# Kernel optimization log

Measured on AMD Instinct MI355X. Metric: run time of the kernel, lower is better.

## Reference

```python
import jax, jax.numpy as jnp
import numpy as np

B, S, D, H, T = 16, 512, 512, 8, 8
DK = D // H
SCALE = float(1.0 / np.sqrt(DK))
EPS = 1e-5


def setup_inputs() -> dict:
    key = jax.random.key(0)
    ks = jax.random.split(key, 12)
    s = float(1.0 / np.sqrt(D))  # torch Linear default init scale
    u = lambda k, shp: jax.random.uniform(k, shp, jnp.float32, -s, s)
    return {
        "x": jax.random.normal(ks[0], (B, S, D), jnp.float32),
        "x_type": jax.random.randint(ks[1], (B, S), 0, T, jnp.int32),
        "mask": jax.random.randint(ks[2], (B, S, S), 0, 2, jnp.int32),
        "Wq": u(ks[3], (T, D, D)), "bq": u(ks[4], (T, D)),
        "Wk": u(ks[5], (T, D, D)), "bk": u(ks[6], (T, D)),
        "Wv": u(ks[7], (T, D, D)), "bv": u(ks[8], (T, D)),
        "Wa": u(ks[9], (T, D, D)), "ba": u(ks[10], (T, D)),
        "gamma": jnp.ones((T, D), jnp.float32),
        "beta": jnp.zeros((T, D), jnp.float32),
    }


def _typed_proj(xf, t, W, b):
    # per-node-type linear 'experts': compute all T projections, select by type id
    # xf: [N, D], W: [T, D, D], b: [T, D], t: [N] -> [N, D]
    all_p = jnp.einsum('nd,tdh->nth', xf, W) + b[None]  # [N, T, D]
    return jnp.take_along_axis(all_p, t[:, None, None], axis=1)[:, 0]


def reference(x, x_type, mask, Wq, bq, Wk, bk, Wv, bv, Wa, ba, gamma, beta):
    xf = x.reshape(-1, D)          # [N, D], N = B*S
    t = x_type.reshape(-1)         # [N]

    # heterogeneous Q/K/V dispatch
    q = _typed_proj(xf, t, Wq, bq).reshape(B, S, H, DK).transpose(0, 2, 1, 3)
    k = _typed_proj(xf, t, Wk, bk).reshape(B, S, H, DK).transpose(0, 2, 1, 3)
    v = _typed_proj(xf, t, Wv, bv).reshape(B, S, H, DK).transpose(0, 2, 1, 3)

    # scaled dot-product attention with boolean mask (mask==0 -> -1e9)
    scores = jnp.einsum('bhqd,bhkd->bhqk', q, k) * SCALE  # [B, H, S, S]
    scores = jnp.where(mask[:, None] == 0, jnp.float32(-1e9), scores)
    p = jax.nn.softmax(scores, axis=-1)
    att = jnp.einsum('bhqk,bhkd->bhqd', p, v)             # [B, H, S, DK]
    att = att.transpose(0, 2, 1, 3).reshape(-1, D)        # [N, D]

    # per-type output projection + residual + per-type LayerNorm
    a = _typed_proj(att, t, Wa, ba)
    h = a + xf
    mu = jnp.mean(h, axis=-1, keepdims=True)
    var = jnp.mean((h - mu) ** 2, axis=-1, keepdims=True)
    out = (h - mu) * jax.lax.rsqrt(var + EPS) * gamma[t] + beta[t]
    return out.reshape(B, S, D)
```

## Files before the change

### kernel.cpp

```cpp
#include <hip/hip_runtime.h>
#include <hip/hip_bf16.h>

typedef __attribute__((ext_vector_type(8))) short short8;
typedef __attribute__((ext_vector_type(4))) float f32x4;
typedef __attribute__((ext_vector_type(4))) unsigned short u16x4;
typedef unsigned short u16;
typedef unsigned int u32;
typedef unsigned long long u64;

#define NB 16
#define NS 512
#define ND 512
#define NH 8
#define NT 8
#define NDK 64
#define NN (NB*NS)
#define SCALE_LOG2E 0.18033688011112042f
#define BM 128
#define BN 128
#define BKK 64

__device__ __forceinline__ u16 f2bf(float f) {
    __hip_bfloat16 h = __float2bfloat16(f);
    return *reinterpret_cast<u16*>(&h);
}
__device__ __forceinline__ u32 pk2(float lo, float hi) {
    return (u32)f2bf(lo) | ((u32)f2bf(hi) << 16);
}

typedef const __attribute__((address_space(1))) void* gas_t;
typedef __attribute__((address_space(3))) void* las_t;

__device__ __forceinline__ void gload16(const void* gsrc, void* ldst) {
    __builtin_amdgcn_global_load_lds((gas_t)gsrc, (las_t)ldst, 16, 0, 0);
}

__global__ __launch_bounds__(256) void bucketize(
    const int* __restrict__ xty, int* __restrict__ perm, int* __restrict__ typeoff,
    int* __restrict__ tile_type, int* __restrict__ tile_row0, int* __restrict__ ntiles)
{
    __shared__ int cnt[NT], off[NT + 1], cur[NT];
    int tid = threadIdx.x;
    if (tid < NT) cnt[tid] = 0;
    __syncthreads();
    for (int n = tid; n < NN; n += 256) atomicAdd(&cnt[xty[n]], 1);
    __syncthreads();
    if (tid == 0) {
        int acc = 0, nt = 0;
        for (int t = 0; t < NT; ++t) {
            off[t] = acc;
            for (int r = 0; r < cnt[t]; r += BM) { tile_type[nt] = t; tile_row0[nt] = acc + r; ++nt; }
            acc += cnt[t];
        }
        off[NT] = acc;
        *ntiles = nt;
        for (int t = 0; t <= NT; ++t) typeoff[t] = off[t];
    }
    __syncthreads();
    if (tid < NT) cur[tid] = off[tid];
    __syncthreads();
    for (int n = tid; n < NN; n += 256) {
        int t = xty[n];
        int p = atomicAdd(&cur[t], 1);
        perm[p] = n;
    }
}

__global__ __launch_bounds__(256) void cvt_x(const float* __restrict__ x, u16* __restrict__ xb)
{
    int i = blockIdx.x * 256 + threadIdx.x;
    float4 v = reinterpret_cast<const float4*>(x)[i];
    u16x4 o;
    o.x = f2bf(v.x); o.y = f2bf(v.y); o.z = f2bf(v.z); o.w = f2bf(v.w);
    reinterpret_cast<u16x4*>(xb)[i] = o;
}

__global__ __launch_bounds__(256) void cvt_w(
    const float* __restrict__ Wq, const float* __restrict__ Wk,
    const float* __restrict__ Wv, const float* __restrict__ Wa,
    u16* __restrict__ Wqt, u16* __restrict__ Wkt, u16* __restrict__ Wvt, u16* __restrict__ Wat)
{
    int arr = blockIdx.z >> 3, t = blockIdx.z & 7;
    const float* W = (arr == 0 ? Wq : arr == 1 ? Wk : arr == 2 ? Wv : Wa) + ((size_t)t << 18);
    u16* O = (arr == 0 ? Wqt : arr == 1 ? Wkt : arr == 2 ? Wvt : Wat) + ((size_t)t << 18);
    int d0 = blockIdx.x * 64, h0 = blockIdx.y * 64;
    __shared__ __align__(16) float tile[64][68];
    int tx = threadIdx.x & 15, ty = threadIdx.x >> 4;
    #pragma unroll
    for (int i = 0; i < 4; ++i) {
        int r = ty + i * 16;
        float4 v = *reinterpret_cast<const float4*>(&W[(size_t)(d0 + r) * ND + h0 + tx * 4]);
        *reinterpret_cast<float4*>(&tile[r][tx * 4]) = v;
    }
    __syncthreads();
    #pragma unroll
    for (int i = 0; i < 4; ++i) {
        int r = ty + i * 16;
        u16x4 o;
        o.x = f2bf(tile[tx * 4 + 0][r]);
        o.y = f2bf(tile[tx * 4 + 1][r]);
        o.z = f2bf(tile[tx * 4 + 2][r]);
        o.w = f2bf(tile[tx * 4 + 3][r]);
        *reinterpret_cast<u16x4*>(&O[(size_t)(h0 + r) * ND + d0 + tx * 4]) = o;
    }
}

__global__ __launch_bounds__(256) void pack_mask(const int* __restrict__ mask, u64* __restrict__ maskb)
{
    int i = blockIdx.x * 256 + threadIdx.x;
    int v = mask[i];
    u64 bal = __ballot(v != 0);
    if ((threadIdx.x & 63) == 0) maskb[i >> 6] = bal;
}

__global__ __launch_bounds__(256) void qkv_gemm(
    const u16* __restrict__ xb,
    const u16* __restrict__ Wqt, const u16* __restrict__ Wkt, const u16* __restrict__ Wvt,
    const float* __restrict__ bq, const float* __restrict__ bk, const float* __restrict__ bv,
    const int* __restrict__ perm, const int* __restrict__ typeoff,
    const int* __restrict__ tile_type, const int* __restrict__ tile_row0, const int* __restrict__ ntiles,
    u16* __restrict__ qb, u16* __restrict__ kbf, u16* __restrict__ vb)
{
    int work = (blockIdx.x & 7) * 108 + (blockIdx.x >> 3);
    int tile = work / 12, pc = work % 12;
    if (tile >= *ntiles) return;
    int t = tile_type[tile];
    int row0 = tile_row0[tile];
    int rows = typeoff[t + 1] - row0; if (rows > BM) rows = BM;
    int proj = pc >> 2;
    int col0 = (pc & 3) * BN;
    const u16* W = (proj == 0 ? Wqt : proj == 1 ? Wkt : Wvt) + ((size_t)t << 18);
    const float* bias = (proj == 0 ? bq : proj == 1 ? bk : bv) + (t << 9);
    u16* outp = proj == 0 ? qb : proj == 1 ? kbf : vb;
    float qscale = proj == 0 ? SCALE_LOG2E : 1.f;

    __shared__ __align__(16) u16 As[2][BM][BKK];
    __shared__ __align__(16) u16 Bs[2][BM][BKK];
    __shared__ int stok[BM];

    int tid = threadIdx.x;
    if (tid < BM) stok[tid] = perm[row0 + (tid < rows ? tid : 0)];
    __syncthreads();

    int lane = tid & 63, w = tid >> 6;
    int wr = w >> 1, wc = w & 1;
    int fr = lane & 15, g = lane >> 4;

    int lrow = lane >> 3;
    int schunk = (lane & 7) ^ lrow;
    int tokA[4];
    #pragma unroll
    for (int k = 0; k < 4; ++k) tokA[k] = stok[w * 32 + k * 8 + lrow];

    auto stage = [&](int buf, int k0) {
        #pragma unroll
        for (int k = 0; k < 4; ++k) {
            gload16(xb + (((size_t)tokA[k]) << 9) + k0 + schunk * 8, &As[buf][w * 32 + k * 8][0]);
            gload16(W + (((size_t)(col0 + w * 32 + k * 8 + lrow)) << 9) + k0 + schunk * 8,
                    &Bs[buf][w * 32 + k * 8][0]);
        }
    };

    f32x4 acc[4][4] = {};

    stage(0, 0);
    #pragma unroll
    for (int it = 0; it < 8; ++it) {
        int cur = it & 1;
        if (it < 7) {
            stage(cur ^ 1, (it + 1) * BKK);
            asm volatile("s_waitcnt vmcnt(8)" ::: "memory");
        } else {
            asm volatile("s_waitcnt vmcnt(0)" ::: "memory");
        }
        __builtin_amdgcn_s_barrier();

        const char* Ab = (const char*)As[cur];
        const char* Bb = (const char*)Bs[cur];
        #pragma unroll
        for (int ks = 0; ks < 2; ++ks) {
            short8 af[4], bfr[4];
            #pragma unroll
            for (int m = 0; m < 4; ++m) {
                int r = wr * 64 + m * 16 + fr;
                af[m] = *reinterpret_cast<const short8*>(Ab + r * 128 + (((ks * 4 + g) ^ (r & 7)) << 4));
            }
            #pragma unroll
            for (int n = 0; n < 4; ++n) {
                int r = wc * 64 + n * 16 + fr;
                bfr[n] = *reinterpret_cast<const short8*>(Bb + r * 128 + (((ks * 4 + g) ^ (r & 7)) << 4));
            }
            #pragma unroll
            for (int m = 0; m < 4; ++m)
                #pragma unroll
                for (int n = 0; n < 4; ++n)
                    acc[m][n] = __builtin_amdgcn_mfma_f32_16x16x32_bf16(af[m], bfr[n], acc[m][n], 0, 0, 0);
        }
        asm volatile("s_waitcnt lgkmcnt(0)" ::: "memory");
        __builtin_amdgcn_s_barrier();
    }

    int rbase = g << 2;
    #pragma unroll
    for (int n = 0; n < 4; ++n) {
        int c = col0 + wc * 64 + n * 16 + fr;
        float bv_ = bias[c];
        int h = c >> 6, dk = c & 63;
        #pragma unroll
        for (int m = 0; m < 4; ++m) {
            #pragma unroll
            for (int i = 0; i < 4; ++i) {
                int r = wr * 64 + m * 16 + rbase + i;
                if (r < rows) {
                    int tok = stok[r];
                    int b = tok >> 9, s = tok & 511;
                    outp[((size_t)((b * NH + h) * NS + s) << 6) + dk] =
                        f2bf((acc[m][n][i] + bv_) * qscale);
                }
            }
        }
    }
}

__global__ __launch_bounds__(256) void transp_v(const u16* __restrict__ vb, u16* __restrict__ vtb)
{
    int bh = blockIdx.y, s0 = blockIdx.x * 64;
    __shared__ __align__(16) u16 t[64][72];
    int tid = threadIdx.x;
    const u16* src = vb + ((size_t)bh << 15) + ((size_t)s0 << 6);
    #pragma unroll
    for (int it = 0; it < 2; ++it) {
        int idx = it * 256 + tid;
        int s = idx & 63, c = idx >> 6;
        short8 v = *reinterpret_cast<const short8*>(src + ((size_t)s << 6) + c * 8);
        #pragma unroll
        for (int j = 0; j < 8; ++j) t[c * 8 + j][s] = ((const u16*)&v)[j];
    }
    __syncthreads();
    u16* dst = vtb + ((size_t)bh << 15) + s0;
    #pragma unroll
    for (int it = 0; it < 2; ++it) {
        int idx = it * 256 + tid;
        int dk = idx >> 3, c = idx & 7;
        short8 v = *reinterpret_cast<const short8*>(&t[dk][c * 8]);
        *reinterpret_cast<short8*>(dst + (size_t)dk * NS + c * 8) = v;
    }
}

__global__ __launch_bounds__(256) void attn_mfma(
    const u16* __restrict__ qb, const u16* __restrict__ kbf, const u16* __restrict__ vtb,
    const u64* __restrict__ maskb, u16* __restrict__ attb)
{
    int work = (blockIdx.x & 7) * 128 + (blockIdx.x >> 3);
    int bh = work >> 3, jq = work & 7;
    int b = bh >> 3, h = bh & 7;
    int q0 = jq * 64;
    int tid = threadIdx.x, lane = tid & 63, w = tid >> 6;
    int ln15 = lane & 15, g = lane >> 4;

    __shared__ __align__(16) u16 sK[64 * 64];
    __shared__ __align__(16) u16 sVt[64 * 64];
    __shared__ __align__(16) u16 sP[4 * 16 * 68];

    const u16* Qg = qb + ((size_t)(bh * NS + q0 + w * 16 + ln15) << 6);
    short8 aq0 = *reinterpret_cast<const short8*>(Qg + g * 8);
    short8 aq1 = *reinterpret_cast<const short8*>(Qg + 32 + g * 8);

    const u16* Kg = kbf + ((size_t)bh << 15);
    const u16* Vtg = vtb + ((size_t)bh << 15);
    int srow = tid >> 3, schunk = tid & 7;

    const u64* Mq = maskb + ((size_t)((b << 9) + q0 + w * 16 + ln15)) * 8;
    float mrun = -3.0e38f, lrun = 0.f;
    f32x4 acc_o[4] = {};

    short8 kpre0 = *reinterpret_cast<const short8*>(Kg + ((size_t)srow << 6) + schunk * 8);
    short8 kpre1 = *reinterpret_cast<const short8*>(Kg + ((size_t)(srow + 32) << 6) + schunk * 8);
    short8 vpre0 = *reinterpret_cast<const short8*>(Vtg + (size_t)srow * NS + schunk * 8);
    short8 vpre1 = *reinterpret_cast<const short8*>(Vtg + (size_t)(srow + 32) * NS + schunk * 8);

    char* sPw = (char*)sP + w * 16 * 136;

    for (int j = 0; j < 8; ++j) {
        __syncthreads();
        {
            int r2 = srow + 32;
            *reinterpret_cast<short8*>((char*)sK  + srow * 128 + ((schunk * 16) ^ ((srow & 7) << 4))) = kpre0;
            *reinterpret_cast<short8*>((char*)sK  + r2   * 128 + ((schunk * 16) ^ ((r2   & 7) << 4))) = kpre1;
            *reinterpret_cast<short8*>((char*)sVt + srow * 128 + ((schunk * 16) ^ ((srow & 7) << 4))) = vpre0;
            *reinterpret_cast<short8*>((char*)sVt + r2   * 128 + ((schunk * 16) ^ ((r2   & 7) << 4))) = vpre1;
        }
        if (j < 7) {
            int j1 = j + 1;
            kpre0 = *reinterpret_cast<const short8*>(Kg + ((size_t)(j1 * 64 + srow) << 6) + schunk * 8);
            kpre1 = *reinterpret_cast<const short8*>(Kg + ((size_t)(j1 * 64 + srow + 32) << 6) + schunk * 8);
            vpre0 = *reinterpret_cast<const short8*>(Vtg + (size_t)srow * NS + j1 * 64 + schunk * 8);
            vpre1 = *reinterpret_cast<const short8*>(Vtg + (size_t)(srow + 32) * NS + j1 * 64 + schunk * 8);
        }
        __syncthreads();

        f32x4 accs[4] = {};
        #pragma unroll
        for (int ks = 0; ks < 2; ++ks) {
            short8 bq_ = ks ? aq1 : aq0;
            #pragma unroll
            for (int n = 0; n < 4; ++n) {
                int row = n * 16 + ln15;
                short8 kfrag = *reinterpret_cast<const short8*>(
                    (char*)sK + row * 128 + (((ks * 64) + g * 16) ^ ((row & 7) << 4)));
                accs[n] = __builtin_amdgcn_mfma_f32_16x16x32_bf16(kfrag, bq_, accs[n], 0, 0, 0);
            }
        }

        u64 mw = Mq[j];
        float sv[4][4];
        float mx = -3.0e38f;
        #pragma unroll
        for (int n = 0; n < 4; ++n) {
            u32 b4 = (u32)(mw >> (n * 16 + g * 4)) & 15u;
            #pragma unroll
            for (int r = 0; r < 4; ++r) {
                float s = (b4 >> r) & 1u ? accs[n][r] : -1.0e9f;
                sv[n][r] = s;
                mx = fmaxf(mx, s);
            }
        }
        mx = fmaxf(mx, __shfl_xor(mx, 16));
        mx = fmaxf(mx, __shfl_xor(mx, 32));

        if (__any(mx > mrun + 8.f)) {
            float nm = fmaxf(mrun, mx);
            float sc = exp2f(mrun - nm);
            mrun = nm;
            lrun *= sc;
            #pragma unroll
            for (int i = 0; i < 4; ++i) {
                float si = __shfl(sc, g * 4 + i);
                #pragma unroll
                for (int n2 = 0; n2 < 4; ++n2) acc_o[n2][i] *= si;
            }
        }

        float ps = 0.f;
        #pragma unroll
        for (int n = 0; n < 4; ++n) {
            float p0 = exp2f(sv[n][0] - mrun), p1 = exp2f(sv[n][1] - mrun);
            float p2 = exp2f(sv[n][2] - mrun), p3 = exp2f(sv[n][3] - mrun);
            ps += (p0 + p1) + (p2 + p3);
            *reinterpret_cast<u32*>(sPw + ln15 * 136 + n * 32 + g * 8 + 0) = pk2(p0, p1);
            *reinterpret_cast<u32*>(sPw + ln15 * 136 + n * 32 + g * 8 + 4) = pk2(p2, p3);
        }
        ps += __shfl_xor(ps, 16);
        ps += __shfl_xor(ps, 32);
        lrun += ps;

        #pragma unroll
        for (int ks = 0; ks < 2; ++ks) {
            short8 ap = *reinterpret_cast<const short8*>(sPw + ln15 * 136 + ks * 64 + g * 16);
            #pragma unroll
            for (int n2 = 0; n2 < 4; ++n2) {
                int row = n2 * 16 + ln15;
                short8 vfrag = *reinterpret_cast<const short8*>(
                    (char*)sVt + row * 128 + (((ks * 64) + g * 16) ^ ((row & 7) << 4)));
                acc_o[n2] = __builtin_amdgcn_mfma_f32_16x16x32_bf16(ap, vfrag, acc_o[n2], 0, 0, 0);
            }
        }
    }

    float linv = 1.f / lrun;
    #pragma unroll
    for (int i = 0; i < 4; ++i) {
        float li = __shfl(linv, g * 4 + i);
        int q = q0 + w * 16 + g * 4 + i;
        #pragma unroll
        for (int n2 = 0; n2 < 4; ++n2) {
            attb[((size_t)((b << 9) + q) << 9) + (h << 6) + n2 * 16 + ln15] =
                f2bf(acc_o[n2][i] * li);
        }
    }
}

__global__ __launch_bounds__(256) void out_gemm(
    const u16* __restrict__ attb, const u16* __restrict__ Wat, const float* __restrict__ ba,
    const int* __restrict__ perm, const int* __restrict__ typeoff,
    const int* __restrict__ tile_type, const int* __restrict__ tile_row0, const int* __restrict__ ntiles,
    const float* __restrict__ x, float* __restrict__ hbuf)
{
    int work = (blockIdx.x & 7) * 36 + (blockIdx.x >> 3);
    int tile = work >> 2;
    if (tile >= *ntiles) return;
    int t = tile_type[tile];
    int row0 = tile_row0[tile];
    int rows = typeoff[t + 1] - row0; if (rows > BM) rows = BM;
    int col0 = (work & 3) * BN;
    const u16* W = Wat + ((size_t)t << 18);
    const float* bias = ba + (t << 9);

    __shared__ __align__(16) u16 As[2][BM][BKK];
    __shared__ __align__(16) u16 Bs[2][BM][BKK];
    __shared__ int stok[BM];

    int tid = threadIdx.x;
    if (tid < BM) stok[tid] = perm[row0 + (tid < rows ? tid : 0)];
    __syncthreads();

    int lane = tid & 63, w = tid >> 6;
    int wr = w >> 1, wc = w & 1;
    int fr = lane & 15, g = lane >> 4;

    int lrow = lane >> 3;
    int schunk = (lane & 7) ^ lrow;
    int tokA[4];
    #pragma unroll
    for (int k = 0; k < 4; ++k) tokA[k] = stok[w * 32 + k * 8 + lrow];

    auto stage = [&](int buf, int k0) {
        #pragma unroll
        for (int k = 0; k < 4; ++k) {
            gload16(attb + (((size_t)tokA[k]) << 9) + k0 + schunk * 8, &As[buf][w * 32 + k * 8][0]);
            gload16(W + (((size_t)(col0 + w * 32 + k * 8 + lrow)) << 9) + k0 + schunk * 8,
                    &Bs[buf][w * 32 + k * 8][0]);
        }
    };

    f32x4 acc[4][4] = {};

    stage(0, 0);
    #pragma unroll
    for (int it = 0; it < 8; ++it) {
        int cur = it & 1;
        if (it < 7) {
            stage(cur ^ 1, (it + 1) * BKK);
            asm volatile("s_waitcnt vmcnt(8)" ::: "memory");
        } else {
            asm volatile("s_waitcnt vmcnt(0)" ::: "memory");
        }
        __builtin_amdgcn_s_barrier();

        const char* Ab = (const char*)As[cur];
        const char* Bb = (const char*)Bs[cur];
        #pragma unroll
        for (int ks = 0; ks < 2; ++ks) {
            short8 af[4], bfr[4];
            #pragma unroll
            for (int m = 0; m < 4; ++m) {
                int r = wr * 64 + m * 16 + fr;
                af[m] = *reinterpret_cast<const short8*>(Ab + r * 128 + (((ks * 4 + g) ^ (r & 7)) << 4));
            }
            #pragma unroll
            for (int n = 0; n < 4; ++n) {
                int r = wc * 64 + n * 16 + fr;
                bfr[n] = *reinterpret_cast<const short8*>(Bb + r * 128 + (((ks * 4 + g) ^ (r & 7)) << 4));
            }
            #pragma unroll
            for (int m = 0; m < 4; ++m)
                #pragma unroll
                for (int n = 0; n < 4; ++n)
                    acc[m][n] = __builtin_amdgcn_mfma_f32_16x16x32_bf16(af[m], bfr[n], acc[m][n], 0, 0, 0);
        }
        asm volatile("s_waitcnt lgkmcnt(0)" ::: "memory");
        __builtin_amdgcn_s_barrier();
    }

    int rbase = g << 2;
    #pragma unroll
    for (int n = 0; n < 4; ++n) {
        int c = col0 + wc * 64 + n * 16 + fr;
        float bv_ = bias[c];
        #pragma unroll
        for (int m = 0; m < 4; ++m) {
            #pragma unroll
            for (int i = 0; i < 4; ++i) {
                int r = wr * 64 + m * 16 + rbase + i;
                if (r < rows) {
                    int tok = stok[r];
                    size_t off = (size_t)tok * ND + c;
                    hbuf[off] = acc[m][n][i] + bv_ + x[off];
                }
            }
        }
    }
}

__global__ __launch_bounds__(256) void lnorm(
    const float* __restrict__ hbuf, const int* __restrict__ xty,
    const float* __restrict__ gamma, const float* __restrict__ beta, float* __restrict__ out)
{
    int row = blockIdx.x * 4 + (threadIdx.x >> 6);
    int lane = threadIdx.x & 63;
    const float4* h4 = reinterpret_cast<const float4*>(hbuf + (size_t)row * ND);
    float4 a = h4[lane * 2], b = h4[lane * 2 + 1];
    float sum = a.x + a.y + a.z + a.w + b.x + b.y + b.z + b.w;
    float sq = a.x * a.x + a.y * a.y + a.z * a.z + a.w * a.w
             + b.x * b.x + b.y * b.y + b.z * b.z + b.w * b.w;
    #pragma unroll
    for (int off = 32; off; off >>= 1) { sum += __shfl_xor(sum, off); sq += __shfl_xor(sq, off); }
    float mu = sum * (1.f / ND);
    float var = sq * (1.f / ND) - mu * mu;
    float is = rsqrtf(var + 1e-5f);
    int t = xty[row];
    const float4* g4 = reinterpret_cast<const float4*>(gamma + ((size_t)t << 9));
    const float4* be4 = reinterpret_cast<const float4*>(beta + ((size_t)t << 9));
    float4 g0 = g4[lane * 2], g1 = g4[lane * 2 + 1];
    float4 b0 = be4[lane * 2], b1 = be4[lane * 2 + 1];
    float4 o0, o1;
    o0.x = (a.x - mu) * is * g0.x + b0.x;
    o0.y = (a.y - mu) * is * g0.y + b0.y;
    o0.z = (a.z - mu) * is * g0.z + b0.z;
    o0.w = (a.w - mu) * is * g0.w + b0.w;
    o1.x = (b.x - mu) * is * g1.x + b1.x;
    o1.y = (b.y - mu) * is * g1.y + b1.y;
    o1.z = (b.z - mu) * is * g1.z + b1.z;
    o1.w = (b.w - mu) * is * g1.w + b1.w;
    float4* out4 = reinterpret_cast<float4*>(out + (size_t)row * ND);
    out4[lane * 2] = o0; out4[lane * 2 + 1] = o1;
}

extern "C" void kernel_launch(void* const* d_in, const int* in_sizes, int n_in,
                              void* d_out, int out_size, void* d_ws, size_t ws_size,
                              hipStream_t stream)
{
    const float* x     = (const float*)d_in[0];
    const int*   xty   = (const int*)d_in[1];
    const int*   mask  = (const int*)d_in[2];
    const float* Wq    = (const float*)d_in[3];
    const float* bq    = (const float*)d_in[4];
    const float* Wk    = (const float*)d_in[5];
    const float* bk    = (const float*)d_in[6];
    const float* Wv    = (const float*)d_in[7];
    const float* bv    = (const float*)d_in[8];
    const float* Wa    = (const float*)d_in[9];
    const float* ba    = (const float*)d_in[10];
    const float* gamma = (const float*)d_in[11];
    const float* beta  = (const float*)d_in[12];
    float* out = (float*)d_out;

    char* ws = (char*)d_ws;
    u16*   xb      = (u16*)(ws + 0);
    u16*   Wqt     = (u16*)(ws + 8388608);
    u16*   Wkt     = (u16*)(ws + 12582912);
    u16*   Wvt     = (u16*)(ws + 16777216);
    u16*   Wat     = (u16*)(ws + 20971520);
    u16*   qb      = (u16*)(ws + 25165824);
    u16*   kbf     = (u16*)(ws + 33554432);
    u16*   vb      = (u16*)(ws + 41943040);
    u16*   vtb     = (u16*)(ws + 50331648);
    u16*   attb    = (u16*)(ws + 58720256);
    float* hbuf    = (float*)(ws + 67108864);
    u64*   maskb   = (u64*)(ws + 83886080);
    int*   perm    = (int*)(ws + 84410368);
    int*   typeoff = (int*)(ws + 84443136);
    int*   ttile   = (int*)(ws + 84443200);
    int*   trow    = (int*)(ws + 84443520);
    int*   ntiles  = (int*)(ws + 84443840);

    bucketize<<<dim3(1), dim3(256), 0, stream>>>(xty, perm, typeoff, ttile, trow, ntiles);
    cvt_x<<<dim3(4096), dim3(256), 0, stream>>>(x, xb);
    cvt_w<<<dim3(8, 8, 32), dim3(256), 0, stream>>>(Wq, Wk, Wv, Wa, Wqt, Wkt, Wvt, Wat);
    pack_mask<<<dim3(16384), dim3(256), 0, stream>>>(mask, maskb);
    qkv_gemm<<<dim3(864), dim3(256), 0, stream>>>(xb, Wqt, Wkt, Wvt, bq, bk, bv,
                                                  perm, typeoff, ttile, trow, ntiles, qb, kbf, vb);
    transp_v<<<dim3(8, 128), dim3(256), 0, stream>>>(vb, vtb);
    attn_mfma<<<dim3(1024), dim3(256), 0, stream>>>(qb, kbf, vtb, maskb, attb);
    out_gemm<<<dim3(288), dim3(256), 0, stream>>>(attb, Wat, ba,
                                                  perm, typeoff, ttile, trow, ntiles, x, hbuf);
    lnorm<<<dim3(2048), dim3(256), 0, stream>>>(hbuf, xty, gamma, beta, out);
}
```

Measured before the change: 270.9 us.

## Fuse preprocessing kernels, parallelize bucketize, stage QKV epilogue through LDS, add setprio

Merges the x conversion, weight transpose-conversion, mask packing and per-segment type counting into one kernel. The single-block bucketize is replaced by a 64-block two-phase count-and-scatter. The QKV GEMM epilogue now stages results in shared memory and writes 128-byte contiguous rows instead of scattered 2-byte stores. MFMA sections in attention are wrapped with s_setprio. The trade-offs are an extra memset and a more complex prefix computation, and the scatter order within a type is no longer deterministic.

```diff
diff --git a/kernel.cpp b/kernel.cpp
--- a/kernel.cpp
+++ b/kernel.cpp
@@ -35,82 +35,106 @@
     __builtin_amdgcn_global_load_lds((gas_t)gsrc, (las_t)ldst, 16, 0, 0);
 }
 
-__global__ __launch_bounds__(256) void bucketize(
-    const int* __restrict__ xty, int* __restrict__ perm, int* __restrict__ typeoff,
+__global__ __launch_bounds__(256) void pre_all(
+    const float* __restrict__ x, const int* __restrict__ xty, const int* __restrict__ mask,
+    const float* __restrict__ Wq, const float* __restrict__ Wk,
+    const float* __restrict__ Wv, const float* __restrict__ Wa,
+    u16* __restrict__ xb,
+    u16* __restrict__ Wqt, u16* __restrict__ Wkt, u16* __restrict__ Wvt, u16* __restrict__ Wat,
+    u64* __restrict__ maskb, int* __restrict__ gcnt, int* __restrict__ scnt)
+{
+    __shared__ __align__(16) float tile[64][68];
+    __shared__ int cnt[NT];
+    int bid = blockIdx.x, tid = threadIdx.x;
+
+    if (bid < 4096) {
+        int i = bid * 256 + tid;
+        float4 v = reinterpret_cast<const float4*>(x)[i];
+        u16x4 o;
+        o.x = f2bf(v.x); o.y = f2bf(v.y); o.z = f2bf(v.z); o.w = f2bf(v.w);
+        reinterpret_cast<u16x4*>(xb)[i] = o;
+    } else if (bid < 6144) {
+        int wid = bid - 4096;
+        int bx = wid & 7, by = (wid >> 3) & 7, bz = wid >> 6;
+        int arr = bz >> 3, t = bz & 7;
+        const float* W = (arr == 0 ? Wq : arr == 1 ? Wk : arr == 2 ? Wv : Wa) + ((size_t)t << 18);
+        u16* O = (arr == 0 ? Wqt : arr == 1 ? Wkt : arr == 2 ? Wvt : Wat) + ((size_t)t << 18);
+        int d0 = bx * 64, h0 = by * 64;
+        int tx = tid & 15, ty = tid >> 4;
+        #pragma unroll
+        for (int i = 0; i < 4; ++i) {
+            int r = ty + i * 16;
+            float4 v = *reinterpret_cast<const float4*>(&W[(size_t)(d0 + r) * ND + h0 + tx * 4]);
+            *reinterpret_cast<float4*>(&tile[r][tx * 4]) = v;
+        }
+        __syncthreads();
+        #pragma unroll
+        for (int i = 0; i < 4; ++i) {
+            int r = ty + i * 16;
+            u16x4 o;
+            o.x = f2bf(tile[tx * 4 + 0][r]);
+            o.y = f2bf(tile[tx * 4 + 1][r]);
+            o.z = f2bf(tile[tx * 4 + 2][r]);
+            o.w = f2bf(tile[tx * 4 + 3][r]);
+            *reinterpret_cast<u16x4*>(&O[(size_t)(h0 + r) * ND + d0 + tx * 4]) = o;
+        }
+    } else if (bid < 7168) {
+        int base = (bid - 6144) * 16;
+        #pragma unroll
+        for (int c = 0; c < 16; ++c) {
+            int i = (base + c) * 256 + tid;
+            int v = mask[i];
+            u64 bal = __ballot(v != 0);
+            if ((tid & 63) == 0) maskb[i >> 6] = bal;
+        }
+    } else {
+        int s = bid - 7168;
+        if (tid < NT) cnt[tid] = 0;
+        __syncthreads();
+        if (tid < 128) atomicAdd(&cnt[xty[s * 128 + tid]], 1);
+        __syncthreads();
+        if (tid < NT) {
+            scnt[s * 8 + tid] = cnt[tid];
+            atomicAdd(&gcnt[tid], cnt[tid]);
+        }
+    }
+}
+
+__global__ __launch_bounds__(256) void scatter_k(
+    const int* __restrict__ xty, const int* __restrict__ gcnt, const int* __restrict__ scnt,
+    int* __restrict__ perm, int* __restrict__ typeoff,
     int* __restrict__ tile_type, int* __restrict__ tile_row0, int* __restrict__ ntiles)
 {
-    __shared__ int cnt[NT], off[NT + 1], cur[NT];
-    int tid = threadIdx.x;
-    if (tid < NT) cnt[tid] = 0;
+    __shared__ int base[NT];
+    int s = blockIdx.x, tid = threadIdx.x;
+    if (tid < NT) {
+        int off = 0;
+        for (int tt = 0; tt < tid; ++tt) off += gcnt[tt];
+        base[tid] = off;
+    }
     __syncthreads();
-    for (int n = tid; n < NN; n += 256) atomicAdd(&cnt[xty[n]], 1);
+    {
+        int t = tid & 7;
+        for (int ss = tid >> 3; ss < s; ss += 32) atomicAdd(&base[t], scnt[ss * 8 + t]);
+    }
     __syncthreads();
-    if (tid == 0) {
+    if (tid < 128) {
+        int n = s * 128 + tid;
+        int t = xty[n];
+        int p = atomicAdd(&base[t], 1);
+        perm[p] = n;
+    }
+    if (s == 0 && tid == 0) {
         int acc = 0, nt = 0;
         for (int t = 0; t < NT; ++t) {
-            off[t] = acc;
-            for (int r = 0; r < cnt[t]; r += BM) { tile_type[nt] = t; tile_row0[nt] = acc + r; ++nt; }
-            acc += cnt[t];
-        }
-        off[NT] = acc;
+            typeoff[t] = acc;
+            int c = gcnt[t];
+            for (int r = 0; r < c; r += BM) { tile_type[nt] = t; tile_row0[nt] = acc + r; ++nt; }
+            acc += c;
+        }
+        typeoff[NT] = acc;
         *ntiles = nt;
-        for (int t = 0; t <= NT; ++t) typeoff[t] = off[t];
-    }
-    __syncthreads();
-    if (tid < NT) cur[tid] = off[tid];
-    __syncthreads();
-    for (int n = tid; n < NN; n += 256) {
-        int t = xty[n];
-        int p = atomicAdd(&cur[t], 1);
-        perm[p] = n;
-    }
-}
-
-__global__ __launch_bounds__(256) void cvt_x(const float* __restrict__ x, u16* __restrict__ xb)
-{
-    int i = blockIdx.x * 256 + threadIdx.x;
-    float4 v = reinterpret_cast<const float4*>(x)[i];
-    u16x4 o;
-    o.x = f2bf(v.x); o.y = f2bf(v.y); o.z = f2bf(v.z); o.w = f2bf(v.w);
-    reinterpret_cast<u16x4*>(xb)[i] = o;
-}
-
-__global__ __launch_bounds__(256) void cvt_w(
-    const float* __restrict__ Wq, const float* __restrict__ Wk,
-    const float* __restrict__ Wv, const float* __restrict__ Wa,
-    u16* __restrict__ Wqt, u16* __restrict__ Wkt, u16* __restrict__ Wvt, u16* __restrict__ Wat)
-{
-    int arr = blockIdx.z >> 3, t = blockIdx.z & 7;
-    const float* W = (arr == 0 ? Wq : arr == 1 ? Wk : arr == 2 ? Wv : Wa) + ((size_t)t << 18);
-    u16* O = (arr == 0 ? Wqt : arr == 1 ? Wkt : arr == 2 ? Wvt : Wat) + ((size_t)t << 18);
-    int d0 = blockIdx.x * 64, h0 = blockIdx.y * 64;
-    __shared__ __align__(16) float tile[64][68];
-    int tx = threadIdx.x & 15, ty = threadIdx.x >> 4;
-    #pragma unroll
-    for (int i = 0; i < 4; ++i) {
-        int r = ty + i * 16;
-        float4 v = *reinterpret_cast<const float4*>(&W[(size_t)(d0 + r) * ND + h0 + tx * 4]);
-        *reinterpret_cast<float4*>(&tile[r][tx * 4]) = v;
-    }
-    __syncthreads();
-    #pragma unroll
-    for (int i = 0; i < 4; ++i) {
-        int r = ty + i * 16;
-        u16x4 o;
-        o.x = f2bf(tile[tx * 4 + 0][r]);
-        o.y = f2bf(tile[tx * 4 + 1][r]);
-        o.z = f2bf(tile[tx * 4 + 2][r]);
-        o.w = f2bf(tile[tx * 4 + 3][r]);
-        *reinterpret_cast<u16x4*>(&O[(size_t)(h0 + r) * ND + d0 + tx * 4]) = o;
-    }
-}
-
-__global__ __launch_bounds__(256) void pack_mask(const int* __restrict__ mask, u64* __restrict__ maskb)
-{
-    int i = blockIdx.x * 256 + threadIdx.x;
-    int v = mask[i];
-    u64 bal = __ballot(v != 0);
-    if ((threadIdx.x & 63) == 0) maskb[i >> 6] = bal;
+    }
 }
 
 __global__ __launch_bounds__(256) void qkv_gemm(
@@ -134,9 +158,9 @@
     u16* outp = proj == 0 ? qb : proj == 1 ? kbf : vb;
     float qscale = proj == 0 ? SCALE_LOG2E : 1.f;
 
-    __shared__ __align__(16) u16 As[2][BM][BKK];
-    __shared__ __align__(16) u16 Bs[2][BM][BKK];
+    __shared__ __align__(16) u16 smem[2][2][BM][BKK];
     __shared__ int stok[BM];
+    auto As = smem[0]; auto Bs = smem[1];
 
     int tid = threadIdx.x;
     if (tid < BM) stok[tid] = perm[row0 + (tid < rows ? tid : 0)];
@@ -200,25 +224,27 @@
         __builtin_amdgcn_s_barrier();
     }
 
-    int rbase = g << 2;
+    u16 (*sT)[136] = reinterpret_cast<u16 (*)[136]>(&smem[0][0][0][0]);
     #pragma unroll
     for (int n = 0; n < 4; ++n) {
-        int c = col0 + wc * 64 + n * 16 + fr;
-        float bv_ = bias[c];
-        int h = c >> 6, dk = c & 63;
-        #pragma unroll
-        for (int m = 0; m < 4; ++m) {
-            #pragma unroll
-            for (int i = 0; i < 4; ++i) {
-                int r = wr * 64 + m * 16 + rbase + i;
-                if (r < rows) {
-                    int tok = stok[r];
-                    int b = tok >> 9, s = tok & 511;
-                    outp[((size_t)((b * NH + h) * NS + s) << 6) + dk] =
-                        f2bf((acc[m][n][i] + bv_) * qscale);
-                }
-            }
-        }
+        int col = wc * 64 + n * 16 + fr;
+        float bv_ = bias[col0 + col];
+        #pragma unroll
+        for (int m = 0; m < 4; ++m)
+            #pragma unroll
+            for (int i = 0; i < 4; ++i)
+                sT[wr * 64 + m * 16 + g * 4 + i][col] = f2bf((acc[m][n][i] + bv_) * qscale);
+    }
+    __syncthreads();
+    int r = tid >> 1, half = tid & 1;
+    if (r < rows) {
+        int tok = stok[r], b = tok >> 9, s = tok & 511;
+        int h = (col0 >> 6) + half;
+        u16* dst = outp + ((size_t)((b * NH + h) * NS + s) << 6);
+        #pragma unroll
+        for (int j = 0; j < 8; ++j)
+            *reinterpret_cast<short8*>(dst + j * 8) =
+                *reinterpret_cast<const short8*>(&sT[r][half * 64 + j * 8]);
     }
 }
 
@@ -300,6 +326,7 @@
         __syncthreads();
 
         f32x4 accs[4] = {};
+        __builtin_amdgcn_s_setprio(1);
         #pragma unroll
         for (int ks = 0; ks < 2; ++ks) {
             short8 bq_ = ks ? aq1 : aq0;
@@ -311,6 +338,7 @@
                 accs[n] = __builtin_amdgcn_mfma_f32_16x16x32_bf16(kfrag, bq_, accs[n], 0, 0, 0);
             }
         }
+        __builtin_amdgcn_s_setprio(0);
 
         u64 mw = Mq[j];
         float sv[4][4];
@@ -354,6 +382,7 @@
         ps += __shfl_xor(ps, 32);
         lrun += ps;
 
+        __builtin_amdgcn_s_setprio(1);
         #pragma unroll
         for (int ks = 0; ks < 2; ++ks) {
             short8 ap = *reinterpret_cast<const short8*>(sPw + ln15 * 136 + ks * 64 + g * 16);
@@ -365,6 +394,7 @@
                 acc_o[n2] = __builtin_amdgcn_mfma_f32_16x16x32_bf16(ap, vfrag, acc_o[n2], 0, 0, 0);
             }
         }
+        __builtin_amdgcn_s_setprio(0);
     }
 
     float linv = 1.f / lrun;
@@ -551,13 +581,15 @@
     int*   perm    = (int*)(ws + 84410368);
     int*   typeoff = (int*)(ws + 84443136);
     int*   ttile   = (int*)(ws + 84443200);
-    int*   trow    = (int*)(ws + 84443520);
-    int*   ntiles  = (int*)(ws + 84443840);
-
-    bucketize<<<dim3(1), dim3(256), 0, stream>>>(xty, perm, typeoff, ttile, trow, ntiles);
-    cvt_x<<<dim3(4096), dim3(256), 0, stream>>>(x, xb);
-    cvt_w<<<dim3(8, 8, 32), dim3(256), 0, stream>>>(Wq, Wk, Wv, Wa, Wqt, Wkt, Wvt, Wat);
-    pack_mask<<<dim3(16384), dim3(256), 0, stream>>>(mask, maskb);
+    int*   trow    = (int*)(ws + 84443776);
+    int*   ntiles  = (int*)(ws + 84444352);
+    int*   gcnt    = (int*)(ws + 84444416);
+    int*   scnt    = (int*)(ws + 84444480);
+
+    hipMemsetAsync(gcnt, 0, 32, stream);
+    pre_all<<<dim3(7232), dim3(256), 0, stream>>>(x, xty, mask, Wq, Wk, Wv, Wa,
+                                                  xb, Wqt, Wkt, Wvt, Wat, maskb, gcnt, scnt);
+    scatter_k<<<dim3(64), dim3(256), 0, stream>>>(xty, gcnt, scnt, perm, typeoff, ttile, trow, ntiles);
     qkv_gemm<<<dim3(864), dim3(256), 0, stream>>>(xb, Wqt, Wkt, Wvt, bq, bk, bv,
                                                   perm, typeoff, ttile, trow, ntiles, qb, kbf, vb);
     transp_v<<<dim3(8, 128), dim3(256), 0, stream>>>(vb, vtb);
```

After: 251.1 us. -7.3%, faster.
